# Optimization experiments

Hardware: AMD Instinct MI355X
Metric: run time of the kernel (lower is better)

## Reference

```python
import jax, jax.numpy as jnp
import numpy as np

N_QUBITS = 4
N_LAYERS = 2
DIM = 1 << N_QUBITS  # 16-dim state vector

# --- fixed (parameter-free) CNOT entangler layers, precomputed as 16x16 permutations ---

def _cnot_perm(c, t):
    M = np.zeros((DIM, DIM), np.complex64)
    for b in range(DIM):
        b2 = b ^ (1 << (N_QUBITS - 1 - t)) if (b >> (N_QUBITS - 1 - c)) & 1 else b
        M[b2, b] = 1.0
    return M

def _entangler(r):
    E = np.eye(DIM, dtype=np.complex64)
    for i in range(N_QUBITS):  # pennylane applies CNOT(i, (i+r)%n) sequentially
        E = _cnot_perm(i, (i + r) % N_QUBITS) @ E
    return E

ENT = [jnp.asarray(_entangler((l % (N_QUBITS - 1)) + 1)) for l in range(N_LAYERS)]
# Z_TABLE[b, w] = <b| Z_w |b>
Z_TABLE = jnp.asarray(np.array([[1.0 - 2.0 * ((b >> (N_QUBITS - 1 - w)) & 1) for w in range(N_QUBITS)] for b in range(DIM)], np.float32))


def _rot(phi, theta, omega):
    # pennylane Rot = RZ(omega) @ RY(theta) @ RZ(phi)
    c = jnp.cos(theta / 2).astype(jnp.complex64)
    s = jnp.sin(theta / 2).astype(jnp.complex64)
    a = jnp.exp(-0.5j * (phi + omega)) * c
    b = -jnp.exp(0.5j * (phi - omega)) * s
    cc = jnp.exp(-0.5j * (phi - omega)) * s
    d = jnp.exp(0.5j * (phi + omega)) * c
    return jnp.stack([jnp.stack([a, b]), jnp.stack([cc, d])])


def _vqc_unitary(weights):
    # weights: [N_LAYERS, N_QUBITS, 3] -> 16x16 unitary for StronglyEntanglingLayers
    U = jnp.eye(DIM, dtype=jnp.complex64)
    for l in range(N_LAYERS):
        R = _rot(weights[l, 0, 0], weights[l, 0, 1], weights[l, 0, 2])
        for q in range(1, N_QUBITS):  # wire 0 is most-significant bit -> left kron factor
            R = jnp.kron(R, _rot(weights[l, q, 0], weights[l, q, 1], weights[l, q, 2]))
        U = ENT[l] @ (R @ U)
    return U


def _vqc(x, weights):
    # x: [..., 4] rotation angles; AngleEmbedding uses RX: RX(a)|0> = [cos(a/2), -i sin(a/2)]
    c = jnp.cos(x / 2).astype(jnp.complex64)
    s = jnp.sin(x / 2).astype(jnp.complex64)
    amp = jnp.stack([c, -1j * s], axis=-1)  # [..., 4, 2]
    psi0 = jnp.einsum('...a,...b,...c,...d->...abcd', amp[..., 0, :], amp[..., 1, :], amp[..., 2, :], amp[..., 3, :])
    psi0 = psi0.reshape(x.shape[:-1] + (DIM,))
    U = _vqc_unitary(weights)
    psi = jnp.einsum('ij,...j->...i', U, psi0)
    probs = psi.real ** 2 + psi.imag ** 2
    return probs @ Z_TABLE  # [..., 4] PauliZ expectation values


def setup_inputs() -> dict:
    key = jax.random.key(0)
    k0, k1, k2, k3 = jax.random.split(key, 4)
    H = 768
    B, S = 8, 2048
    embeddings = jax.random.normal(k0, (B, S, H), dtype=jnp.float32)
    lim = 1.0 / np.sqrt(H)
    Wq = jax.random.normal(k1, (N_QUBITS, H), dtype=jnp.float32) * lim
    Wk = jax.random.normal(k2, (N_QUBITS, H), dtype=jnp.float32) * lim
    bq = jnp.zeros((N_QUBITS,), jnp.float32)
    bk = jnp.zeros((N_QUBITS,), jnp.float32)
    vqc_weights = jax.random.uniform(k3, (N_LAYERS, N_QUBITS, 3), dtype=jnp.float32) * (2.0 * np.pi)
    return {'embeddings': embeddings, 'Wq': Wq, 'bq': bq, 'Wk': Wk, 'bk': bk, 'vqc_weights': vqc_weights}


def reference(embeddings, Wq, bq, Wk, bk, vqc_weights):
    Q = jnp.einsum('bsh,qh->bsq', embeddings, Wq) + bq  # [B,S,4]
    K = jnp.einsum('bsh,qh->bsq', embeddings, Wk) + bk
    Qv = _vqc(Q, vqc_weights)  # [B,S,4]
    Kv = _vqc(K, vqc_weights)
    attn = jax.nn.softmax(jnp.einsum('bsq,btq->bst', Qv, Kv), axis=-1)  # [B,S,S]
    return jnp.einsum('bst,bth->bsh', attn, embeddings)
```

## Files before the change

kernel.cpp:

```cpp
#include <hip/hip_runtime.h>

#define NB 8
#define NS 2048
#define NH 768
#define NPOS (NB*NS)

typedef _Float16 half8 __attribute__((ext_vector_type(8)));
typedef float floatx4 __attribute__((ext_vector_type(4)));

#define GLOAD_LDS16(gp, lp) __builtin_amdgcn_global_load_lds( \
  (const __attribute__((address_space(1))) unsigned int*)(gp), \
  (__attribute__((address_space(3))) unsigned int*)(lp), 16, 0, 0)

__global__ __launch_bounds__(384) void epre_kernel(
    const float* __restrict__ E, const float* __restrict__ wts,
    float* __restrict__ Vre, float* __restrict__ Vim,
    unsigned short* __restrict__ ET) {
  int tc = blockIdx.x, hb = blockIdx.y, b = blockIdx.z;
  int tid = threadIdx.x;

  if (tc == 0 && hb == 0 && b == 0 && tid < 16) {
    int j = tid;
    float ar[16], ai[16];
#pragma unroll
    for (int i = 0; i < 16; i++) { ar[i] = (i == j) ? 1.f : 0.f; ai[i] = 0.f; }
#pragma unroll
    for (int l = 0; l < 2; l++) {
#pragma unroll
      for (int q = 0; q < 4; q++) {
        float phi = wts[(l*4+q)*3+0];
        float th  = wts[(l*4+q)*3+1];
        float om  = wts[(l*4+q)*3+2];
        float ct = cosf(0.5f*th), st = sinf(0.5f*th);
        float sm = 0.5f*(phi+om), df = 0.5f*(phi-om);
        float cs = cosf(sm), ss = sinf(sm), cd = cosf(df), sd = sinf(df);
        float Ar =  cs*ct, Ai = -ss*ct;
        float Br = -cd*st, Bi = -sd*st;
        float Cr =  cd*st, Ci = -sd*st;
        float Dr =  cs*ct, Di =  ss*ct;
        int pb = 1 << (3-q);
#pragma unroll
        for (int b0 = 0; b0 < 16; b0++) {
          if (b0 & pb) continue;
          int b1 = b0 | pb;
          float xr = ar[b0], xi = ai[b0], yr = ar[b1], yi = ai[b1];
          ar[b0] = Ar*xr - Ai*xi + Br*yr - Bi*yi;
          ai[b0] = Ar*xi + Ai*xr + Br*yi + Bi*yr;
          ar[b1] = Cr*xr - Ci*xi + Dr*yr - Di*yi;
          ai[b1] = Cr*xi + Ci*xr + Dr*yi + Di*yr;
        }
      }
      const int r = (l == 0) ? 1 : 2;
#pragma unroll
      for (int i2 = 0; i2 < 4; i2++) {
        int cb = 1 << (3-i2);
        int tb = 1 << (3-((i2+r)&3));
#pragma unroll
        for (int b0 = 0; b0 < 16; b0++) {
          if ((b0 & cb) && !(b0 & tb)) {
            int b1 = b0 | tb;
            float tr = ar[b0], ti = ai[b0];
            ar[b0] = ar[b1]; ai[b0] = ai[b1];
            ar[b1] = tr;     ai[b1] = ti;
          }
        }
      }
    }
    int pc = __popc((unsigned)j) & 3;
#pragma unroll
    for (int i = 0; i < 16; i++) {
      float vr = ar[i], vi = ai[i], orr, oi;
      if      (pc == 0) { orr =  vr; oi =  vi; }
      else if (pc == 1) { orr =  vi; oi = -vr; }
      else if (pc == 2) { orr = -vr; oi = -vi; }
      else              { orr = -vi; oi =  vr; }
      Vre[i*16+j] = orr;
      Vim[i*16+j] = oi;
    }
  }

  size_t tbase = ((size_t)((b*4 + hb)*64 + tc)) * 12288;
  const float* Eb = E + (size_t)b*NS*NH + (size_t)tc*32*NH + hb*192;
#pragma unroll
  for (int u = 0; u < 2; u++) {
    int unit = tid + 384*u;
    int q2 = unit / 192, h2 = unit % 192;
    unsigned hi4[4], lo4[4];
#pragma unroll
    for (int jp = 0; jp < 4; jp++) {
      float ea = Eb[(size_t)(q2*8 + 2*jp    )*NH + h2];
      float eb = Eb[(size_t)(q2*8 + 2*jp + 1)*NH + h2];
      _Float16 ha = (_Float16)ea, hb16 = (_Float16)eb;
      float la = ea - (float)ha, lb = eb - (float)hb16;
      unsigned uha = __builtin_bit_cast(unsigned short, ha);
      unsigned uhb = __builtin_bit_cast(unsigned short, hb16);
      unsigned ula = __builtin_bit_cast(unsigned short, (_Float16)la);
      unsigned ulb = __builtin_bit_cast(unsigned short, (_Float16)lb);
      hi4[jp] = uha | (uhb << 16);
      lo4[jp] = ula | (ulb << 16);
    }
    int off = h2*32 + ((q2 ^ ((h2>>1)&3))*8);
    *(uint4*)&ET[tbase + off]        = make_uint4(hi4[0],hi4[1],hi4[2],hi4[3]);
    *(uint4*)&ET[tbase + 6144 + off] = make_uint4(lo4[0],lo4[1],lo4[2],lo4[3]);
  }
}

__global__ __launch_bounds__(256) void proj_vqc_kernel(
    const float* __restrict__ E, const float* __restrict__ Wq, const float* __restrict__ bq,
    const float* __restrict__ Wk, const float* __restrict__ bk,
    const float* __restrict__ Vre, const float* __restrict__ Vim,
    float* __restrict__ Qv, float* __restrict__ Kv) {
  __shared__ __align__(16) float WqL[768*4];
  __shared__ __align__(16) float WkL[768*4];
  __shared__ float Vsh[2][16*17];
  int tid = threadIdx.x;
  for (int idx = tid; idx < 768*4; idx += 256) {
    int e = idx >> 2, w = idx & 3;
    WqL[e*4+w] = Wq[w*768+e];
    WkL[e*4+w] = Wk[w*768+e];
  }
  if (tid < 256) {
    int i = tid >> 4, jj = tid & 15;
    Vsh[0][i*17+jj] = Vre[tid];
    Vsh[1][i*17+jj] = Vim[tid];
  }
  __syncthreads();
  float bqr0=bq[0], bqr1=bq[1], bqr2=bq[2], bqr3=bq[3];
  float bkr0=bk[0], bkr1=bk[1], bkr2=bk[2], bkr3=bk[3];
  int lane = tid & 63;
  int wid  = blockIdx.x*4 + (tid >> 6);
  int nw   = gridDim.x*4;
  int grp  = lane >> 4;
  int i    = lane & 15;
  for (int pos = wid; pos < NPOS; pos += nw) {
    const float* er = E + (size_t)pos*768;
    float pq[4] = {0.f,0.f,0.f,0.f};
    float pk[4] = {0.f,0.f,0.f,0.f};
#pragma unroll
    for (int k2 = 0; k2 < 3; k2++) {
      float4 ev = *(const float4*)(er + lane*4 + 256*k2);
#pragma unroll
      for (int jj = 0; jj < 4; jj++) {
        int e = lane*4 + 256*k2 + jj;
        float evs = (jj==0) ? ev.x : (jj==1) ? ev.y : (jj==2) ? ev.z : ev.w;
        float4 wq4 = *(const float4*)&WqL[e*4];
        float4 wk4 = *(const float4*)&WkL[e*4];
        pq[0] += evs*wq4.x; pq[1] += evs*wq4.y; pq[2] += evs*wq4.z; pq[3] += evs*wq4.w;
        pk[0] += evs*wk4.x; pk[1] += evs*wk4.y; pk[2] += evs*wk4.z; pk[3] += evs*wk4.w;
      }
    }
    float part[8];
#pragma unroll
    for (int w = 0; w < 8; w++) {
      float v = (w < 4) ? pq[w] : pk[w-4];
      v += __shfl_xor(v, 32); v += __shfl_xor(v, 16); v += __shfl_xor(v, 8);
      v += __shfl_xor(v, 4);  v += __shfl_xor(v, 2);  v += __shfl_xor(v, 1);
      part[w] = v;
    }
    if (grp < 2) {
      float a0,a1,a2,a3;
      if (grp == 0) { a0=part[0]+bqr0; a1=part[1]+bqr1; a2=part[2]+bqr2; a3=part[3]+bqr3; }
      else          { a0=part[4]+bkr0; a1=part[5]+bkr1; a2=part[6]+bkr2; a3=part[7]+bkr3; }
      float c0=cosf(0.5f*a0), s0=sinf(0.5f*a0);
      float c1=cosf(0.5f*a1), s1=sinf(0.5f*a1);
      float c2=cosf(0.5f*a2), s2=sinf(0.5f*a2);
      float c3=cosf(0.5f*a3), s3=sinf(0.5f*a3);
      float m[16];
#pragma unroll
      for (int j2 = 0; j2 < 16; j2++) {
        float f0 = (j2 & 8) ? s0 : c0;
        float f1 = (j2 & 4) ? s1 : c1;
        float f2 = (j2 & 2) ? s2 : c2;
        float f3 = (j2 & 1) ? s3 : c3;
        m[j2] = f0*f1*f2*f3;
      }
      float re = 0.f, im = 0.f;
#pragma unroll
      for (int j2 = 0; j2 < 16; j2++) {
        re += Vsh[0][i*17+j2]*m[j2];
        im += Vsh[1][i*17+j2]*m[j2];
      }
      float pr = re*re + im*im;
      float r0 = (i & 8) ? -pr : pr;
      float r1 = (i & 4) ? -pr : pr;
      float r2 = (i & 2) ? -pr : pr;
      float r3 = (i & 1) ? -pr : pr;
#pragma unroll
      for (int off = 8; off >= 1; off >>= 1) {
        r0 += __shfl_xor(r0, off);
        r1 += __shfl_xor(r1, off);
        r2 += __shfl_xor(r2, off);
        r3 += __shfl_xor(r3, off);
      }
      if (i == 0) {
        float* dst = (grp == 0 ? Qv : Kv) + (size_t)pos*4;
        dst[0]=r0; dst[1]=r1; dst[2]=r2; dst[3]=r3;
      }
    }
  }
}

#define TKC 32

__global__ __launch_bounds__(512, 4) void attn_kernel(
    const unsigned short* __restrict__ ET, const float* __restrict__ Qv,
    const float* __restrict__ Kv, float* __restrict__ out) {
  int bid  = blockIdx.x;
  int b    = bid & 7;
  int r    = bid >> 3;
  int sblk = r & 31;
  int hp   = r >> 5;
  int tid  = threadIdx.x;
  int lane = tid & 63;
  int w    = tid >> 6;

  __shared__ __align__(16) unsigned short sA[2][2048];
  __shared__ __align__(16) unsigned short sB[24576];
  __shared__ float dfin[64];

  const unsigned short* tEh = ET + ((size_t)((b*4 + hp*2)*64)) * 12288;

  int sPg  = tid >> 3;
  int half = tid & 7;
  int og   = half >> 1;
  int sub  = half & 1;
  int qg   = og ^ ((sPg >> 1) & 3);
  int offA = sPg*32 + og*8 + sub*4;
  float4 qv = *(const float4*)&Qv[((size_t)(b*NS + sblk*64) + sPg)*4];
  const float* kvbase = Kv + (size_t)b*NS*4 + (size_t)(qg*8 + sub*4)*4;
  float den_acc = 0.f;

  floatx4 acc[4][3];
#pragma unroll
  for (int i = 0; i < 4; i++)
#pragma unroll
    for (int jt = 0; jt < 3; jt++) acc[i][jt] = floatx4{0.f,0.f,0.f,0.f};

  int m16 = lane & 15, q16 = lane >> 4;
  int cidx = (q16 ^ ((m16 >> 1) & 3)) * 8;
  int t16 = tid * 8;
  int tileoff = (w >> 2)*12288;
  int hsub = (w & 3)*48;

  auto kvload = [&](int ci, float4* kvr) {
    const float* kvp = kvbase + (size_t)ci*128;
#pragma unroll
    for (int j = 0; j < 4; j++) kvr[j] = *(const float4*)(kvp + j*4);
  };

  auto pcompute = [&](const float4* kvr) -> uint2 {
    float p[4];
    float dsum = 0.f;
#pragma unroll
    for (int j = 0; j < 4; j++) {
      float4 kk = kvr[j];
      float arg = qv.x*kk.x + qv.y*kk.y + qv.z*kk.z + qv.w*kk.w;
      p[j] = __expf(arg);
      dsum += p[j];
    }
    den_acc += dsum;
    unsigned u0 = (unsigned)__builtin_bit_cast(unsigned short, (_Float16)p[0])
                | ((unsigned)__builtin_bit_cast(unsigned short, (_Float16)p[1]) << 16);
    unsigned u1 = (unsigned)__builtin_bit_cast(unsigned short, (_Float16)p[2])
                | ((unsigned)__builtin_bit_cast(unsigned short, (_Float16)p[3]) << 16);
    return make_uint2(u0, u1);
  };

  auto dma_chunk = [&](int ci) {
    const unsigned short* t0 = tEh + (size_t)ci*12288;
    const unsigned short* t1 = t0 + (size_t)64*12288;
    GLOAD_LDS16(t0 + t16,        sB + t16);
    GLOAD_LDS16(t0 + 4096 + t16, sB + 4096 + t16);
    GLOAD_LDS16(t0 + 8192 + t16, sB + 8192 + t16);
    GLOAD_LDS16(t1 + t16,        sB + 12288 + t16);
    GLOAD_LDS16(t1 + 4096 + t16, sB + 16384 + t16);
    GLOAD_LDS16(t1 + 8192 + t16, sB + 20480 + t16);
  };

  {
    float4 kvr[4];
    kvload(0, kvr);
    dma_chunk(0);
    uint2 ph = pcompute(kvr);
    *(uint2*)&sA[0][offA] = ph;
  }

  for (int ci = 0; ci < 64; ci++) {
    int cb = ci & 1;
    uint2 ph;
    if (ci < 63) {
      float4 kvr[4];
      kvload(ci+1, kvr);
      ph = pcompute(kvr);
    }
    __syncthreads();
    if (ci > 0) dma_chunk(ci);
    if (ci < 63) *(uint2*)&sA[cb^1][offA] = ph;
    __syncthreads();

    const unsigned short* sAc = &sA[cb][0];
    half8 a[4];
#pragma unroll
    for (int i = 0; i < 4; i++) {
      int srow = i*16 + m16;
      a[i] = __builtin_bit_cast(half8, *(const uint4*)&sAc[srow*TKC + cidx]);
    }
#pragma unroll
    for (int jt = 0; jt < 3; jt++) {
      int ro = tileoff + (hsub + jt*16 + m16)*TKC + cidx;
      half8 bh_ = __builtin_bit_cast(half8, *(const uint4*)&sB[ro]);
      half8 bl_ = __builtin_bit_cast(half8, *(const uint4*)&sB[ro + 6144]);
#pragma unroll
      for (int i = 0; i < 4; i++) {
        acc[i][jt] = __builtin_amdgcn_mfma_f32_16x16x32_f16(a[i], bl_, acc[i][jt], 0, 0, 0);
        acc[i][jt] = __builtin_amdgcn_mfma_f32_16x16x32_f16(a[i], bh_, acc[i][jt], 0, 0, 0);
      }
    }
  }

  {
    float v = den_acc;
    v += __shfl_xor(v, 1);
    v += __shfl_xor(v, 2);
    v += __shfl_xor(v, 4);
    if (half == 0) dfin[sPg] = v;
  }
  __syncthreads();

  float* ob = out + ((size_t)(b*NS + sblk*64))*NH + hp*384;
#pragma unroll
  for (int i = 0; i < 4; i++) {
#pragma unroll
    for (int reg = 0; reg < 4; reg++) {
      int s_loc = i*16 + q16*4 + reg;
      float invd = 1.0f / dfin[s_loc];
#pragma unroll
      for (int jt = 0; jt < 3; jt++) {
        int h_loc = (w >> 2)*192 + hsub + jt*16 + m16;
        ob[(size_t)s_loc*NH + h_loc] = acc[i][jt][reg] * invd;
      }
    }
  }
}

extern "C" void kernel_launch(void* const* d_in, const int* in_sizes, int n_in,
                              void* d_out, int out_size, void* d_ws, size_t ws_size,
                              hipStream_t stream) {
  const float* E   = (const float*)d_in[0];
  const float* Wq  = (const float*)d_in[1];
  const float* bq  = (const float*)d_in[2];
  const float* Wk  = (const float*)d_in[3];
  const float* bk  = (const float*)d_in[4];
  const float* wts = (const float*)d_in[5];
  float* ws  = (float*)d_ws;
  float* Vre = ws;
  float* Vim = ws + 256;
  float* Qv  = ws + 512;
  float* Kv  = Qv + (size_t)NPOS*4;
  unsigned short* ET = (unsigned short*)(Kv + (size_t)NPOS*4);
  float* out = (float*)d_out;

  epre_kernel<<<dim3(64, 4, 8), 384, 0, stream>>>(E, wts, Vre, Vim, ET);
  proj_vqc_kernel<<<1024, 256, 0, stream>>>(E, Wq, bq, Wk, bk, Vre, Vim, Qv, Kv);
  attn_kernel<<<dim3(512), 512, 0, stream>>>(ET, Qv, Kv, out);
}
```

Baseline: 269.7 us.

## Split E tiles into lo/hi LDS buffers to overlap DMA with MFMA

The pre-pass now writes the transposed fp16 embedding tiles so that each 32-row chunk's lo and hi residual images are contiguous per head-pair. The attention kernel keeps separate LDS buffers for the lo and hi parts. The loop computes the lo-part MFMAs while the hi part of the same chunk streams into LDS, then prefetches the next chunk's lo part while computing the hi-part MFMAs. This replaces the old load-everything-then-compute step, which had two barriers per chunk. The goal is to hide global-to-LDS transfer latency behind matrix work without growing LDS, at the cost of a tighter dependency schedule that relies on barriers to drain the async loads.

```diff
diff --git a/kernel.cpp b/kernel.cpp
--- a/kernel.cpp
+++ b/kernel.cpp
@@ -79,7 +79,7 @@
     }
   }
 
-  size_t tbase = ((size_t)((b*4 + hb)*64 + tc)) * 12288;
+  size_t tb2 = ((size_t)((b*2 + (hb>>1))*64 + tc)) * 24576 + (size_t)(hb & 1)*6144;
   const float* Eb = E + (size_t)b*NS*NH + (size_t)tc*32*NH + hb*192;
 #pragma unroll
   for (int u = 0; u < 2; u++) {
@@ -100,8 +100,8 @@
       lo4[jp] = ula | (ulb << 16);
     }
     int off = h2*32 + ((q2 ^ ((h2>>1)&3))*8);
-    *(uint4*)&ET[tbase + off]        = make_uint4(hi4[0],hi4[1],hi4[2],hi4[3]);
-    *(uint4*)&ET[tbase + 6144 + off] = make_uint4(lo4[0],lo4[1],lo4[2],lo4[3]);
+    *(uint4*)&ET[tb2 + off]         = make_uint4(lo4[0],lo4[1],lo4[2],lo4[3]);
+    *(uint4*)&ET[tb2 + 12288 + off] = make_uint4(hi4[0],hi4[1],hi4[2],hi4[3]);
   }
 }
 
@@ -215,10 +215,11 @@
   int w    = tid >> 6;
 
   __shared__ __align__(16) unsigned short sA[2][2048];
-  __shared__ __align__(16) unsigned short sB[24576];
+  __shared__ __align__(16) unsigned short sLo[12288];
+  __shared__ __align__(16) unsigned short sHi[12288];
   __shared__ float dfin[64];
 
-  const unsigned short* tEh = ET + ((size_t)((b*4 + hp*2)*64)) * 12288;
+  const unsigned short* tEh = ET + ((size_t)((b*2 + hp)*64)) * 24576;
 
   int sPg  = tid >> 3;
   int half = tid & 7;
@@ -239,7 +240,7 @@
   int m16 = lane & 15, q16 = lane >> 4;
   int cidx = (q16 ^ ((m16 >> 1) & 3)) * 8;
   int t16 = tid * 8;
-  int tileoff = (w >> 2)*12288;
+  int imgoff = (w >> 2)*6144;
   int hsub = (w & 3)*48;
 
   auto kvload = [&](int ci, float4* kvr) {
@@ -266,37 +267,35 @@
     return make_uint2(u0, u1);
   };
 
-  auto dma_chunk = [&](int ci) {
-    const unsigned short* t0 = tEh + (size_t)ci*12288;
-    const unsigned short* t1 = t0 + (size_t)64*12288;
-    GLOAD_LDS16(t0 + t16,        sB + t16);
-    GLOAD_LDS16(t0 + 4096 + t16, sB + 4096 + t16);
-    GLOAD_LDS16(t0 + 8192 + t16, sB + 8192 + t16);
-    GLOAD_LDS16(t1 + t16,        sB + 12288 + t16);
-    GLOAD_LDS16(t1 + 4096 + t16, sB + 16384 + t16);
-    GLOAD_LDS16(t1 + 8192 + t16, sB + 20480 + t16);
-  };
-
   {
     float4 kvr[4];
     kvload(0, kvr);
-    dma_chunk(0);
+    const unsigned short* lsrc = tEh;
+    GLOAD_LDS16(lsrc + t16,        sLo + t16);
+    GLOAD_LDS16(lsrc + 4096 + t16, sLo + 4096 + t16);
+    GLOAD_LDS16(lsrc + 8192 + t16, sLo + 8192 + t16);
     uint2 ph = pcompute(kvr);
     *(uint2*)&sA[0][offA] = ph;
   }
 
   for (int ci = 0; ci < 64; ci++) {
     int cb = ci & 1;
+
+    __syncthreads();
+
+    {
+      const unsigned short* hsrc = tEh + (size_t)ci*24576 + 12288;
+      GLOAD_LDS16(hsrc + t16,        sHi + t16);
+      GLOAD_LDS16(hsrc + 4096 + t16, sHi + 4096 + t16);
+      GLOAD_LDS16(hsrc + 8192 + t16, sHi + 8192 + t16);
+    }
+
     uint2 ph;
     if (ci < 63) {
       float4 kvr[4];
       kvload(ci+1, kvr);
       ph = pcompute(kvr);
     }
-    __syncthreads();
-    if (ci > 0) dma_chunk(ci);
-    if (ci < 63) *(uint2*)&sA[cb^1][offA] = ph;
-    __syncthreads();
 
     const unsigned short* sAc = &sA[cb][0];
     half8 a[4];
@@ -307,14 +306,30 @@
     }
 #pragma unroll
     for (int jt = 0; jt < 3; jt++) {
-      int ro = tileoff + (hsub + jt*16 + m16)*TKC + cidx;
-      half8 bh_ = __builtin_bit_cast(half8, *(const uint4*)&sB[ro]);
-      half8 bl_ = __builtin_bit_cast(half8, *(const uint4*)&sB[ro + 6144]);
-#pragma unroll
-      for (int i = 0; i < 4; i++) {
+      int ro = imgoff + (hsub + jt*16 + m16)*TKC + cidx;
+      half8 bl_ = __builtin_bit_cast(half8, *(const uint4*)&sLo[ro]);
+#pragma unroll
+      for (int i = 0; i < 4; i++)
         acc[i][jt] = __builtin_amdgcn_mfma_f32_16x16x32_f16(a[i], bl_, acc[i][jt], 0, 0, 0);
+    }
+    if (ci < 63) *(uint2*)&sA[cb^1][offA] = ph;
+
+    __syncthreads();
+
+    if (ci < 63) {
+      const unsigned short* lsrc = tEh + (size_t)(ci+1)*24576;
+      GLOAD_LDS16(lsrc + t16,        sLo + t16);
+      GLOAD_LDS16(lsrc + 4096 + t16, sLo + 4096 + t16);
+      GLOAD_LDS16(lsrc + 8192 + t16, sLo + 8192 + t16);
+    }
+
+#pragma unroll
+    for (int jt = 0; jt < 3; jt++) {
+      int ro = imgoff + (hsub + jt*16 + m16)*TKC + cidx;
+      half8 bh_ = __builtin_bit_cast(half8, *(const uint4*)&sHi[ro]);
+#pragma unroll
+      for (int i = 0; i < 4; i++)
         acc[i][jt] = __builtin_amdgcn_mfma_f32_16x16x32_f16(a[i], bh_, acc[i][jt], 0, 0, 0);
-      }
     }
   }
 
```

New measurement: 267.8 us. Within noise of the previous version (-0.7%).
